# Performance work log

Measured on AMD Instinct MI355X. Metric: run time of the kernel, lower is better.

The kernel has to match this reference:

```python
import jax, jax.numpy as jnp
import numpy as np

N, E, H, B = 10000, 320000, 256, 128
ATOM_TYPES, BOND_TYPES = 100, 5


def _timestep_embed(t, dim):
    # Sinusoidal timestep embedding, matching the torch _embed_timestep
    half = dim // 2
    freq = jnp.exp(jnp.arange(half, dtype=jnp.float32) * (-np.log(10000.0) / (half - 1)))
    ang = t[:, None] * freq[None, :]  # [B, half]
    return jnp.concatenate([jnp.sin(ang), jnp.cos(ang)], axis=1)  # [B, dim]


def setup_inputs() -> dict:
    key = jax.random.key(0)
    ks = jax.random.split(key, 9)
    s = 0.02
    return {
        "node_features": jax.random.normal(ks[0], (N, H), jnp.float32),
        "pos_pred": jax.random.normal(ks[1], (N, 3), jnp.float32),
        "edge_index": jax.random.randint(ks[2], (2, E), 0, N),
        "batch": jnp.sort(jax.random.randint(ks[3], (N,), 0, B)),
        "t_discrete": jax.random.uniform(ks[4], (B,), jnp.float32) * 1000.0,
        "atom_w1": jax.random.normal(ks[5], (H, H), jnp.float32) * s,
        "atom_b1": jnp.zeros((H,), jnp.float32),
        "atom_w2": jax.random.normal(ks[6], (H, ATOM_TYPES), jnp.float32) * s,
        "atom_b2": jnp.zeros((ATOM_TYPES,), jnp.float32),
        "bond_w1": jax.random.normal(ks[7], (2 * H, H), jnp.float32) * s,
        "bond_b1": jnp.zeros((H,), jnp.float32),
        "bond_w2": jax.random.normal(ks[8], (H, BOND_TYPES), jnp.float32) * s,
        "bond_b2": jnp.zeros((BOND_TYPES,), jnp.float32),
    }


def reference(node_features, pos_pred, edge_index, batch, t_discrete,
              atom_w1, atom_b1, atom_w2, atom_b2,
              bond_w1, bond_b1, bond_w2, bond_b2):
    # timestep embed + per-node broadcast-gather
    t_emb = _timestep_embed(t_discrete, node_features.shape[1])  # [B, H]
    h = node_features + t_emb[batch]  # [N, H]

    # atom denoiser MLP
    atom_logits = jax.nn.relu(h @ atom_w1 + atom_b1) @ atom_w2 + atom_b2  # [N, ATOM_TYPES]

    # gather node pairs, concat, bond denoiser MLP
    row, col = edge_index[0], edge_index[1]
    e = jnp.concatenate([h[row], h[col]], axis=-1)  # [E, 2H]
    bond_logits = jax.nn.relu(e @ bond_w1 + bond_b1) @ bond_w2 + bond_b2  # [E, BOND_TYPES]

    return pos_pred, atom_logits, bond_logits, node_features
```

## Files before the change

kernel.cpp:

```cpp
#include <hip/hip_runtime.h>
#include <hip/hip_bf16.h>

typedef __bf16 bf16x8 __attribute__((ext_vector_type(8)));
typedef float  f32x4  __attribute__((ext_vector_type(4)));

#define N_NODES 10000
#define N_EDGES 320000

#define WS_TEMB   0u
#define WS_H      131072u
#define WS_W1AT   5251072u
#define WS_W2AT   5382144u
#define WS_W1BT   5439488u
#define WS_W2BT   5701632u

__global__ void prep_kernel(const float* __restrict__ aw1, const float* __restrict__ aw2,
                            const float* __restrict__ bw1, const float* __restrict__ bw2,
                            const float* __restrict__ t,
                            __hip_bfloat16* __restrict__ W1a, __hip_bfloat16* __restrict__ W2a,
                            __hip_bfloat16* __restrict__ W1b, __hip_bfloat16* __restrict__ W2b,
                            float* __restrict__ temb)
{
    int blk = blockIdx.x;
    if (blk < 256) {
        int i = blk * 256 + threadIdx.x;
        int n = i >> 8, k = i & 255;
        W1a[i] = __float2bfloat16(aw1[k * 256 + n]);
    } else if (blk < 368) {
        int i = (blk - 256) * 256 + threadIdx.x;
        int n = i >> 8, k = i & 255;
        W2a[i] = __float2bfloat16(n < 100 ? aw2[k * 100 + n] : 0.0f);
    } else if (blk < 880) {
        int i = (blk - 368) * 256 + threadIdx.x;
        int n = i >> 9, k = i & 511;
        W1b[i] = __float2bfloat16(bw1[k * 256 + n]);
    } else if (blk < 896) {
        int i = (blk - 880) * 256 + threadIdx.x;
        int n = i >> 8, k = i & 255;
        W2b[i] = __float2bfloat16(n < 5 ? bw2[k * 5 + n] : 0.0f);
    } else {
        int q = blk - 896;
        int b = q * 2 + (threadIdx.x >> 7);
        int i = threadIdx.x & 127;
        float freq = expf((float)i * (-9.210340371976184f / 127.0f));
        float ang  = t[b] * freq;
        temb[b * 256 + i]       = sinf(ang);
        temb[b * 256 + 128 + i] = cosf(ang);
    }
}

__global__ void h_kernel(const float* __restrict__ nf, const int* __restrict__ batch,
                         const float* __restrict__ temb, __hip_bfloat16* __restrict__ hb,
                         float* __restrict__ out_nf,
                         const float4* __restrict__ pos_src, float4* __restrict__ pos_dst)
{
    int blk = blockIdx.x;
    if (blk >= 1250) {
        int j = (blk - 1250) * 256 + threadIdx.x;
        if (j < 7500) pos_dst[j] = pos_src[j];
        return;
    }
    int i = blk * 256 + threadIdx.x;
    int n = i >> 5;
    int c = (i & 31) << 3;
    const float4* p = (const float4*)(nf + (size_t)n * 256 + c);
    float4 v0 = p[0], v1 = p[1];
    int b = batch[n];
    const float4* q = (const float4*)(temb + (size_t)b * 256 + c);
    float4 t0 = q[0], t1 = q[1];
    union { int4 i4; __hip_bfloat16 h[8]; } u;
    u.h[0] = __float2bfloat16(v0.x + t0.x);
    u.h[1] = __float2bfloat16(v0.y + t0.y);
    u.h[2] = __float2bfloat16(v0.z + t0.z);
    u.h[3] = __float2bfloat16(v0.w + t0.w);
    u.h[4] = __float2bfloat16(v1.x + t1.x);
    u.h[5] = __float2bfloat16(v1.y + t1.y);
    u.h[6] = __float2bfloat16(v1.z + t1.z);
    u.h[7] = __float2bfloat16(v1.w + t1.w);
    *(int4*)((char*)hb + (size_t)n * 512 + (size_t)c * 2) = u.i4;
    float4* o = (float4*)(out_nf + (size_t)n * 256 + c);
    o[0] = v0; o[1] = v1;
}

__device__ __forceinline__ void gload16(const void* g, void* l)
{
    __builtin_amdgcn_global_load_lds(
        (const __attribute__((address_space(1))) unsigned int*)g,
        (__attribute__((address_space(3))) unsigned int*)l, 16, 0, 0);
}

template<int NT, bool GATHER, int N2F, int N2REAL>
__global__ __launch_bounds__(512, 2) void mlp_kernel(
    const __hip_bfloat16* __restrict__ hb,
    const __hip_bfloat16* __restrict__ w1t,
    const __hip_bfloat16* __restrict__ w2t,
    const float* __restrict__ b1,
    const float* __restrict__ b2,
    const int*  __restrict__ eidx,
    int M,
    float* __restrict__ out)
{
    extern __shared__ char lds[];
    const int t   = threadIdx.x;
    const int wid = t >> 6;
    const int l   = t & 63;
    const int wm  = wid >> 2;
    const int wn  = wid & 3;
    const int m0  = blockIdx.x * 256;

    const int swz = (((t & 7) ^ ((t >> 3) & 7)) << 4);

    const char* hbase = (const char*)hb;
    int srcA[4][2];
    #pragma unroll
    for (int i = 0; i < 4; ++i) {
        int am = i * 64 + (t >> 3);
        if (GATHER) {
            int e = m0 + am;
            srcA[i][0] = eidx[e] * 512 + swz;
            srcA[i][1] = eidx[N_EDGES + e] * 512 + swz;
        } else {
            int r = m0 + am; if (r > M - 1) r = M - 1;
            srcA[i][0] = r * 512 + swz;
            srcA[i][1] = srcA[i][0];
        }
    }
    const char* w1base = (const char*)w1t;
    int srcB[4];
    #pragma unroll
    for (int i = 0; i < 4; ++i)
        srcB[i] = (i * 64 + (t >> 3)) * (NT * 128) + swz;

    f32x4 acc[8][4];
    #pragma unroll
    for (int i = 0; i < 8; ++i)
        #pragma unroll
        for (int j = 0; j < 4; ++j) acc[i][j] = f32x4{0.f, 0.f, 0.f, 0.f};

    auto STAGE = [&](int ks, char* buf) {
        int side  = (GATHER && ks >= NT / 2) ? 1 : 0;
        int koffA = (GATHER ? (ks & (NT / 2 - 1)) : ks) * 128;
        #pragma unroll
        for (int i = 0; i < 4; ++i)
            gload16(hbase + (long)(srcA[i][side] + koffA), buf + i * 8192 + wid * 1024);
        int koffB = ks * 128;
        #pragma unroll
        for (int i = 0; i < 4; ++i)
            gload16(w1base + (long)(srcB[i] + koffB), buf + 32768 + i * 8192 + wid * 1024);
    };

    STAGE(0, lds);

    for (int kt = 0; kt < NT; ++kt) {
        __syncthreads();
        if (kt + 1 < NT) STAGE(kt + 1, lds + (((kt + 1) & 1) << 16));
        const char* cur = lds + ((kt & 1) << 16);
        #pragma unroll
        for (int k1 = 0; k1 < 2; ++k1) {
            const int jx = (k1 * 4 + (l >> 4)) ^ (l & 7);
            bf16x8 af[8];
            #pragma unroll
            for (int mi = 0; mi < 8; ++mi) {
                int r = wm * 128 + mi * 16 + (l & 15);
                af[mi] = *(const bf16x8*)(cur + r * 128 + (jx << 4));
            }
            #pragma unroll
            for (int ni = 0; ni < 4; ++ni) {
                int rn = wn * 64 + ni * 16 + (l & 15);
                bf16x8 bfr = *(const bf16x8*)(cur + 32768 + rn * 128 + (jx << 4));
                #pragma unroll
                for (int mi = 0; mi < 8; ++mi)
                    acc[mi][ni] = __builtin_amdgcn_mfma_f32_16x16x32_bf16(af[mi], bfr, acc[mi][ni], 0, 0, 0);
            }
        }
    }

    __syncthreads();
    {
        float b1v[4];
        #pragma unroll
        for (int ni = 0; ni < 4; ++ni) b1v[ni] = b1[wn * 64 + ni * 16 + (l & 15)];
        #pragma unroll
        for (int mi = 0; mi < 8; ++mi)
            #pragma unroll
            for (int ni = 0; ni < 4; ++ni)
                #pragma unroll
                for (int r = 0; r < 4; ++r) {
                    int m = wm * 128 + mi * 16 + (l >> 4) * 4 + r;
                    int n = wn * 64 + ni * 16 + (l & 15);
                    float v = fmaxf(acc[mi][ni][r] + b1v[ni], 0.0f);
                    int byte = m * 512 + ((((n >> 3) ^ (m & 7)) << 4)) + ((n & 7) << 1);
                    *(__hip_bfloat16*)(lds + byte) = __float2bfloat16(v);
                }
    }
    __syncthreads();

    f32x4 acc2[2][N2F];
    #pragma unroll
    for (int i = 0; i < 2; ++i)
        #pragma unroll
        for (int j = 0; j < N2F; ++j) acc2[i][j] = f32x4{0.f, 0.f, 0.f, 0.f};
    const char* w2base = (const char*)w2t;
    #pragma unroll
    for (int ks = 0; ks < 8; ++ks) {
        const int jx2 = (ks * 4 + (l >> 4)) ^ (l & 7);
        bf16x8 a2[2];
        #pragma unroll
        for (int mi2 = 0; mi2 < 2; ++mi2) {
            int r2 = wid * 32 + mi2 * 16 + (l & 15);
            a2[mi2] = *(const bf16x8*)(lds + r2 * 512 + (jx2 << 4));
        }
        #pragma unroll
        for (int nf2 = 0; nf2 < N2F; ++nf2) {
            bf16x8 b2f = *(const bf16x8*)(w2base + (nf2 * 16 + (l & 15)) * 512 + ks * 64 + (l >> 4) * 16);
            #pragma unroll
            for (int mi2 = 0; mi2 < 2; ++mi2)
                acc2[mi2][nf2] = __builtin_amdgcn_mfma_f32_16x16x32_bf16(a2[mi2], b2f, acc2[mi2][nf2], 0, 0, 0);
        }
    }
    #pragma unroll
    for (int nf2 = 0; nf2 < N2F; ++nf2) {
        int n = nf2 * 16 + (l & 15);
        if (n < N2REAL) {
            float b2v = b2[n];
            #pragma unroll
            for (int mi2 = 0; mi2 < 2; ++mi2)
                #pragma unroll
                for (int r = 0; r < 4; ++r) {
                    int gm = m0 + wid * 32 + mi2 * 16 + (l >> 4) * 4 + r;
                    if (gm < M)
                        out[(long)gm * N2REAL + n] = acc2[mi2][nf2][r] + b2v;
                }
        }
    }
}

extern "C" void kernel_launch(void* const* d_in, const int* in_sizes, int n_in,
                              void* d_out, int out_size, void* d_ws, size_t ws_size,
                              hipStream_t stream)
{
    const float* node_features = (const float*)d_in[0];
    const float* pos_pred      = (const float*)d_in[1];
    const int*   edge_index    = (const int*)d_in[2];
    const int*   batch         = (const int*)d_in[3];
    const float* t_disc        = (const float*)d_in[4];
    const float* atom_w1       = (const float*)d_in[5];
    const float* atom_b1       = (const float*)d_in[6];
    const float* atom_w2       = (const float*)d_in[7];
    const float* atom_b2       = (const float*)d_in[8];
    const float* bond_w1       = (const float*)d_in[9];
    const float* bond_b1       = (const float*)d_in[10];
    const float* bond_w2       = (const float*)d_in[11];
    const float* bond_b2       = (const float*)d_in[12];

    char* ws = (char*)d_ws;
    float*          temb = (float*)(ws + WS_TEMB);
    __hip_bfloat16* hbf  = (__hip_bfloat16*)(ws + WS_H);
    __hip_bfloat16* W1at = (__hip_bfloat16*)(ws + WS_W1AT);
    __hip_bfloat16* W2at = (__hip_bfloat16*)(ws + WS_W2AT);
    __hip_bfloat16* W1bt = (__hip_bfloat16*)(ws + WS_W1BT);
    __hip_bfloat16* W2bt = (__hip_bfloat16*)(ws + WS_W2BT);

    float* out      = (float*)d_out;
    float* out_pos  = out;
    float* out_atom = out + 30000;
    float* out_bond = out + 1030000;
    float* out_nf   = out + 2630000;

    prep_kernel<<<960, 256, 0, stream>>>(atom_w1, atom_w2, bond_w1, bond_w2, t_disc,
                                         W1at, W2at, W1bt, W2bt, temb);
    h_kernel<<<1280, 256, 0, stream>>>(node_features, batch, temb, hbf, out_nf,
                                       (const float4*)pos_pred, (float4*)out_pos);
    mlp_kernel<4, false, 7, 100><<<40, 512, 131072, stream>>>(
        hbf, W1at, W2at, atom_b1, atom_b2, nullptr, N_NODES, out_atom);
    mlp_kernel<8, true, 1, 5><<<1250, 512, 131072, stream>>>(
        hbf, W1bt, W2bt, bond_b1, bond_b2, edge_index, N_EDGES, out_bond);
}
```

Measured before the change: 214.6 us.

## Split K-tile staging into half-slices and interleave loads with MFMA phases

Reorganizes the first GEMM main loop into four phases per K tile, each loading a half-set of A or B fragments and issuing a 16-MFMA cluster. Global-to-LDS prefetches for the next tile are split into smaller chunks between phases, with explicit vmcnt/lgkmcnt waits, sched barriers and raised priority around MFMA clusters. The LDS layout changes to 64-byte rows per K half with a new swizzle, and fragment registers drop from 8 A fragments to 4. This is meant to overlap memory traffic with matrix math more finely and reduce register pressure, at the cost of more barriers per tile and fragile manual wait counts.

```diff
diff --git a/kernel.cpp b/kernel.cpp
--- a/kernel.cpp
+++ b/kernel.cpp
@@ -89,6 +89,12 @@
         (__attribute__((address_space(3))) unsigned int*)l, 16, 0, 0);
 }
 
+#define WAIT_V4    asm volatile("s_waitcnt vmcnt(4)" ::: "memory")
+#define WAIT_V0    asm volatile("s_waitcnt vmcnt(0)" ::: "memory")
+#define WAIT_LGKM0 asm volatile("s_waitcnt lgkmcnt(0)" ::: "memory")
+#define SCHEDB     __builtin_amdgcn_sched_barrier(0)
+#define BARRIER    __builtin_amdgcn_s_barrier()
+
 template<int NT, bool GATHER, int N2F, int N2REAL>
 __global__ __launch_bounds__(512, 2) void mlp_kernel(
     const __hip_bfloat16* __restrict__ hb,
@@ -108,28 +114,39 @@
     const int wn  = wid & 3;
     const int m0  = blockIdx.x * 256;
 
-    const int swz = (((t & 7) ^ ((t >> 3) & 7)) << 4);
-
-    const char* hbase = (const char*)hb;
-    int srcA[4][2];
-    #pragma unroll
-    for (int i = 0; i < 4; ++i) {
-        int am = i * 64 + (t >> 3);
+    const int jsw = (((((t & 3) - ((t >> 4) & 3)) & 3) ^ ((t >> 2) & 3)) << 4);
+    const int slotF = (((((l >> 4) ^ (l & 3)) + ((l >> 2) & 3)) & 3) << 4);
+
+    const char* hbase  = (const char*)hb;
+    const char* w1base = (const char*)w1t;
+    long srcA[2][2], srcB[2];
+    #pragma unroll
+    for (int i = 0; i < 2; ++i) {
+        int r = i * 128 + (t >> 2);
         if (GATHER) {
-            int e = m0 + am;
-            srcA[i][0] = eidx[e] * 512 + swz;
-            srcA[i][1] = eidx[N_EDGES + e] * 512 + swz;
+            int e = m0 + r;
+            srcA[i][0] = (long)eidx[e] * 512 + jsw;
+            srcA[i][1] = (long)eidx[N_EDGES + e] * 512 + jsw;
         } else {
-            int r = m0 + am; if (r > M - 1) r = M - 1;
-            srcA[i][0] = r * 512 + swz;
-            srcA[i][1] = srcA[i][0];
-        }
-    }
-    const char* w1base = (const char*)w1t;
-    int srcB[4];
-    #pragma unroll
-    for (int i = 0; i < 4; ++i)
-        srcB[i] = (i * 64 + (t >> 3)) * (NT * 128) + swz;
+            int rr = m0 + r; if (rr > M - 1) rr = M - 1;
+            srcA[i][0] = srcA[i][1] = (long)rr * 512 + jsw;
+        }
+        srcB[i] = (long)(i * 128 + (t >> 2)) * (NT * 128) + jsw;
+    }
+
+    auto stageA = [&](int ks, int k1) {
+        char* d = lds + ((ks & 1) << 16) + k1 * 16384 + wid * 1024;
+        int side = (GATHER && ks >= NT / 2) ? 1 : 0;
+        int koff = (GATHER ? (ks & (NT / 2 - 1)) : ks) * 128 + k1 * 64;
+        gload16(hbase + srcA[0][side] + koff, d);
+        gload16(hbase + srcA[1][side] + koff, d + 8192);
+    };
+    auto stageB = [&](int ks, int k1) {
+        char* d = lds + ((ks & 1) << 16) + 32768 + k1 * 16384 + wid * 1024;
+        long koff = (long)ks * 128 + k1 * 64;
+        gload16(w1base + srcB[0] + koff, d);
+        gload16(w1base + srcB[1] + koff, d + 8192);
+    };
 
     f32x4 acc[8][4];
     #pragma unroll
@@ -137,42 +154,59 @@
         #pragma unroll
         for (int j = 0; j < 4; ++j) acc[i][j] = f32x4{0.f, 0.f, 0.f, 0.f};
 
-    auto STAGE = [&](int ks, char* buf) {
-        int side  = (GATHER && ks >= NT / 2) ? 1 : 0;
-        int koffA = (GATHER ? (ks & (NT / 2 - 1)) : ks) * 128;
-        #pragma unroll
-        for (int i = 0; i < 4; ++i)
-            gload16(hbase + (long)(srcA[i][side] + koffA), buf + i * 8192 + wid * 1024);
-        int koffB = ks * 128;
-        #pragma unroll
-        for (int i = 0; i < 4; ++i)
-            gload16(w1base + (long)(srcB[i] + koffB), buf + 32768 + i * 8192 + wid * 1024);
-    };
-
-    STAGE(0, lds);
+    bf16x8 af[4], bfr[4];
+    auto LOAD_AF = [&](const char* base, int k1, int mig) {
+        #pragma unroll
+        for (int a = 0; a < 4; ++a) {
+            int R = wm * 128 + (mig * 4 + a) * 16 + (l & 15);
+            af[a] = *(const bf16x8*)(base + k1 * 16384 + R * 64 + slotF);
+        }
+    };
+    auto LOAD_BFR = [&](const char* base, int k1) {
+        #pragma unroll
+        for (int ni = 0; ni < 4; ++ni) {
+            int R = wn * 64 + ni * 16 + (l & 15);
+            bfr[ni] = *(const bf16x8*)(base + 32768 + k1 * 16384 + R * 64 + slotF);
+        }
+    };
+    auto MFMA16 = [&](int mig) {
+        __builtin_amdgcn_s_setprio(1);
+        #pragma unroll
+        for (int a = 0; a < 4; ++a)
+            #pragma unroll
+            for (int ni = 0; ni < 4; ++ni)
+                acc[mig * 4 + a][ni] =
+                    __builtin_amdgcn_mfma_f32_16x16x32_bf16(af[a], bfr[ni], acc[mig * 4 + a][ni], 0, 0, 0);
+        __builtin_amdgcn_s_setprio(0);
+    };
+
+    stageA(0, 0); stageB(0, 0); stageA(0, 1); stageB(0, 1);
+    WAIT_V4; BARRIER; SCHEDB;
 
     for (int kt = 0; kt < NT; ++kt) {
-        __syncthreads();
-        if (kt + 1 < NT) STAGE(kt + 1, lds + (((kt + 1) & 1) << 16));
         const char* cur = lds + ((kt & 1) << 16);
-        #pragma unroll
-        for (int k1 = 0; k1 < 2; ++k1) {
-            const int jx = (k1 * 4 + (l >> 4)) ^ (l & 7);
-            bf16x8 af[8];
-            #pragma unroll
-            for (int mi = 0; mi < 8; ++mi) {
-                int r = wm * 128 + mi * 16 + (l & 15);
-                af[mi] = *(const bf16x8*)(cur + r * 128 + (jx << 4));
-            }
-            #pragma unroll
-            for (int ni = 0; ni < 4; ++ni) {
-                int rn = wn * 64 + ni * 16 + (l & 15);
-                bf16x8 bfr = *(const bf16x8*)(cur + 32768 + rn * 128 + (jx << 4));
-                #pragma unroll
-                for (int mi = 0; mi < 8; ++mi)
-                    acc[mi][ni] = __builtin_amdgcn_mfma_f32_16x16x32_bf16(af[mi], bfr, acc[mi][ni], 0, 0, 0);
-            }
-        }
+        const bool pf = (kt + 1 < NT);
+        LOAD_AF(cur, 0, 0); LOAD_BFR(cur, 0);
+        if (pf) stageA(kt + 1, 0);
+        BARRIER; WAIT_LGKM0; SCHEDB;
+        MFMA16(0);
+        BARRIER;
+        LOAD_AF(cur, 0, 1);
+        if (pf) stageB(kt + 1, 0);
+        if (pf) { WAIT_V4; } else { WAIT_V0; }
+        BARRIER; WAIT_LGKM0; SCHEDB;
+        MFMA16(1);
+        BARRIER;
+        LOAD_AF(cur, 1, 0); LOAD_BFR(cur, 1);
+        if (pf) stageA(kt + 1, 1);
+        BARRIER; WAIT_LGKM0; SCHEDB;
+        MFMA16(0);
+        BARRIER;
+        LOAD_AF(cur, 1, 1);
+        if (pf) { stageB(kt + 1, 1); WAIT_V4; }
+        BARRIER; WAIT_LGKM0; SCHEDB;
+        MFMA16(1);
+        BARRIER;
     }
 
     __syncthreads();
```

Result: slower. 225.7 us (+5.2%).
